# Performance work log

Hardware: AMD Instinct MI355X
Metric: run time of the kernel (lower is better)

## Reference

```python
import jax, jax.numpy as jnp
import numpy as np

BZ, NA, D, R, H, IN, NACT = 64, 64, 128, 3, 4, 96, 20


def setup_inputs() -> dict:
    key = jax.random.key(0)
    ks = jax.random.split(key, 32)

    def lin(k, out_d, in_d):
        return jax.random.normal(k, (out_d, in_d), jnp.float32) / np.sqrt(in_d)

    def linR(k, out_d, in_d):  # stacked per comm round
        return jax.random.normal(k, (R, out_d, in_d), jnp.float32) / np.sqrt(in_d)

    u = jax.random.uniform(ks[0], (R, BZ, NA, NA, 2), jnp.float32, 1e-6, 1.0 - 1e-6)
    gumbel = -jnp.log(-jnp.log(u))  # gumbel(0,1) noise for gumbel-softmax
    return {
        "obs": jax.random.normal(ks[1], (BZ, NA, IN), jnp.float32),
        "hidden": jax.random.normal(ks[2], (BZ, NA, D), jnp.float32),
        "gumbel": gumbel,
        "W_enc": lin(ks[3], D, IN), "b_enc": jnp.zeros((D,), jnp.float32),
        "W_ih": lin(ks[4], 3 * D, D), "W_hh": lin(ks[5], 3 * D, D),
        "b_ih": jnp.zeros((3 * D,), jnp.float32), "b_hh": jnp.zeros((3 * D,), jnp.float32),
        "W_oth": lin(ks[6], D, D), "b_oth": jnp.zeros((D,), jnp.float32),
        "W_m1": lin(ks[7], D, 2 * D), "b_m1": jnp.zeros((D,), jnp.float32),
        "W_m2": lin(ks[8], D, D), "b_m2": jnp.zeros((D,), jnp.float32),
        "W_s1": linR(ks[9], D // 2, 2 * D), "b_s1": jnp.zeros((R, D // 2), jnp.float32),
        "W_s2": linR(ks[10], 2, D // 2), "b_s2": jnp.zeros((R, 2), jnp.float32),
        "Wq": linR(ks[11], D, D), "Wk": linR(ks[12], D, D),
        "Wv": linR(ks[13], D, D), "Wo": linR(ks[14], D, D),
        "W_q1": lin(ks[15], D, 2 * D), "b_q1": jnp.zeros((D,), jnp.float32),
        "W_q2": lin(ks[16], NACT, D), "b_q2": jnp.zeros((NACT,), jnp.float32),
    }


def reference(obs, hidden, gumbel, W_enc, b_enc, W_ih, W_hh, b_ih, b_hh,
              W_oth, b_oth, W_m1, b_m1, W_m2, b_m2, W_s1, b_s1, W_s2, b_s2,
              Wq, Wk, Wv, Wo, W_q1, b_q1, W_q2, b_q2):
    bz, na, _ = obs.shape
    d = W_enc.shape[0]
    # encoder + GRUCell (single step, pytorch gate order r,z,n)
    x = obs @ W_enc.T + b_enc                      # (bz,na,d)
    gx = x @ W_ih.T + b_ih
    gh = hidden @ W_hh.T + b_hh
    xr, xz, xn = jnp.split(gx, 3, -1)
    hr, hz, hn = jnp.split(gh, 3, -1)
    r = jax.nn.sigmoid(xr + hr)
    z = jax.nn.sigmoid(xz + hz)
    nc = jnp.tanh(xn + r * hn)
    h = (1.0 - z) * nc + z * hidden                # (bz,na,d)
    # others encoder on detached hidden
    others = jax.lax.stop_gradient(h) @ W_oth.T + b_oth
    # all-pairs message: [others_j, self_i] -> 2-layer relu MLP
    others_info = jnp.broadcast_to(others[:, None, :, :], (bz, na, na, d))
    self_info = jnp.broadcast_to(h[:, :, None, :], (bz, na, na, d))
    msg_in = jnp.concatenate([others_info, self_info], -1)   # (bz,na,n,2d)
    message = jax.nn.relu(jax.nn.relu(msg_in @ W_m1.T + b_m1) @ W_m2.T + b_m2)
    sched_in = jnp.concatenate([self_info, message], -1)     # (bz,na,n,2d)
    nH, dk = H, d // H
    scale = 1.0 / np.sqrt(dk)
    results = []
    for i in range(R):
        def sched_mlp(xx):
            return jax.nn.relu(xx @ W_s1[i].T + b_s1[i]) @ W_s2[i].T + b_s2[i]
        # directed: symmetrize over the two agent axes of the MLP input
        logits = 0.5 * sched_mlp(sched_in) + 0.5 * sched_mlp(jnp.swapaxes(sched_in, 1, 2))
        y = logits + gumbel[i]
        y_soft = jax.nn.softmax(y, -1)
        y_hard = jax.nn.one_hot(jnp.argmax(y, -1), 2, dtype=y_soft.dtype)
        y_st = y_hard + y_soft - jax.lax.stop_gradient(y_soft)  # straight-through
        adj = y_st[..., 1]                                      # (bz,na,n)
        # multi-head soft attention of agent i over messages j, masked by adj
        q = (h @ Wq[i].T).reshape(bz, na, nH, dk)
        k = (message @ Wk[i].T).reshape(bz, na, na, nH, dk)
        v = (message @ Wv[i].T).reshape(bz, na, na, nH, dk)
        scores = jnp.einsum('bihe,bijhe->bijh', q, k) * scale   # (bz,na,n,H)
        w = jax.nn.softmax(scores, axis=2) * adj[..., None]
        w = w / (jnp.sum(w, axis=2, keepdims=True) + 1e-10)
        att = jnp.einsum('bijh,bijhe->bihe', w, v).reshape(bz, na, d) @ Wo[i].T
        results.append(jax.nn.elu(att))
    aggre = jnp.mean(jnp.stack(results), 0)
    qout = jnp.concatenate([h, aggre], -1)
    qout = jax.nn.relu(qout @ W_q1.T + b_q1) @ W_q2.T + b_q2
    return qout, h
```

## Files before the change

kernel.cpp:

```cpp
#include <hip/hip_runtime.h>
#include <hip/hip_bf16.h>

typedef __hip_bfloat16 bf16;

#define BZc 64
#define NAc 64
#define Dc 128
#define Rc 3
#define Hc 4
#define INc 96
#define NACTc 20

#define WM1_OFF    0
#define WM2_OFF    16384
#define WS1_OFF    32768
#define WM1ST_OFF  57344
#define WS1ST_OFF  73728
#define WENCT_OFF  98304
#define WIHT_OFF   110592
#define WHHT_OFF   159744
#define WOTHT_OFF  208896
#define WQ1T_OFF   225280
#define WQ2T_OFF   258048
#define MH_OFF     260608
#define P_OFF      457216
#define CHUNK_BASE 655360

__global__ void kW(const float* __restrict__ W_m1, const float* __restrict__ W_m2,
                   const float* __restrict__ W_s1, const float* __restrict__ W_enc,
                   const float* __restrict__ W_ih, const float* __restrict__ W_hh,
                   const float* __restrict__ W_oth, const float* __restrict__ W_q1,
                   const float* __restrict__ W_q2, float* __restrict__ ws) {
  int idx = blockIdx.x * blockDim.x + threadIdx.x;
  if (idx < 16384) {
    int dm = idx & 127, c = idx >> 7;
    ws[WM1_OFF + ((c >> 2) * 128 + dm) * 4 + (c & 3)] = W_m1[dm * 256 + c];
  } else if (idx < 32768) {
    int k = idx - 16384;
    int dm = k & 127, c = k >> 7;
    ws[WM2_OFF + ((c >> 2) * 128 + dm) * 4 + (c & 3)] = W_m2[dm * 128 + c];
  } else if (idx < 57344) {
    int k = idx - 32768;
    int r = k >> 13, rem = k & 8191;
    int du = rem & 63, c = rem >> 6;
    ws[WS1_OFF + r * 8192 + ((c >> 2) * 64 + du) * 4 + (c & 3)] =
        W_s1[(r * 64 + du) * 256 + 128 + c];
  } else if (idx < 73728) {
    int k = idx - 57344;
    int dm = k & 127, c = k >> 7;
    ws[WM1ST_OFF + c * 128 + dm] = W_m1[dm * 256 + 128 + c];
  } else if (idx < 98304) {
    int k = idx - 73728;
    int r = k >> 13, rem = k & 8191;
    int du = rem & 63, c = rem >> 6;
    ws[WS1ST_OFF + r * 8192 + c * 64 + du] = W_s1[(r * 64 + du) * 256 + c];
  } else if (idx < 110592) {
    int k = idx - 98304;
    int o = k & 127, c = k >> 7;
    ws[WENCT_OFF + c * 128 + o] = W_enc[o * 96 + c];
  } else if (idx < 159744) {
    int k = idx - 110592;
    int o = k % 384, c = k / 384;
    ws[WIHT_OFF + c * 384 + o] = W_ih[o * 128 + c];
  } else if (idx < 208896) {
    int k = idx - 159744;
    int o = k % 384, c = k / 384;
    ws[WHHT_OFF + c * 384 + o] = W_hh[o * 128 + c];
  } else if (idx < 225280) {
    int k = idx - 208896;
    int o = k & 127, c = k >> 7;
    ws[WOTHT_OFF + c * 128 + o] = W_oth[o * 128 + c];
  } else if (idx < 258048) {
    int k = idx - 225280;
    int o = k & 127, c = k >> 7;
    ws[WQ1T_OFF + c * 128 + o] = W_q1[o * 256 + c];
  } else if (idx < 260608) {
    int k = idx - 258048;
    int o = k % 20, c = k / 20;
    ws[WQ2T_OFF + c * 20 + o] = W_q2[o * 128 + c];
  }
}

__global__ __launch_bounds__(256) void kMP(
    const float* __restrict__ Wq, const float* __restrict__ Wk,
    const float* __restrict__ Wv, const float* __restrict__ Wo,
    float* __restrict__ Mhq, float* __restrict__ Pq) {
  const int bid = blockIdx.x;
  const int which = bid & 1, hh = (bid >> 1) & 3, r = bid >> 3;
  const int t = threadIdx.x;
  __shared__ float A[4096];
  __shared__ float B[4224];
  if (which == 0) {
    for (int k = t; k < 4096; k += 256) {
      int e = k >> 7, c = k & 127;
      A[k] = Wq[(r * 128 + hh * 32 + e) * 128 + c];
      B[k] = Wk[(r * 128 + hh * 32 + e) * 128 + c];
    }
    __syncthreads();
    for (int k = 0; k < 64; ++k) {
      int o = k * 256 + t, c = o >> 7, d = o & 127;
      float a = 0.f;
      #pragma unroll 8
      for (int e = 0; e < 32; ++e) a += A[e * 128 + c] * B[e * 128 + d];
      Mhq[(size_t)(r * 4 + hh) * 16384 + ((c >> 2) * 128 + d) * 4 + (c & 3)] = a;
    }
  } else {
    for (int k = t; k < 4096; k += 256) A[k] = Wv[(r * 128 + hh * 32 + (k >> 7)) * 128 + (k & 127)];
    for (int k = t; k < 4096; k += 256) {
      int dp = k >> 5, e = k & 31;
      B[dp * 33 + e] = Wo[(r * 128 + dp) * 128 + hh * 32 + e];
    }
    __syncthreads();
    for (int k = 0; k < 64; ++k) {
      int o = k * 256 + t, d = o >> 7, dp = o & 127;
      float a = 0.f;
      #pragma unroll 8
      for (int e = 0; e < 32; ++e) a += A[e * 128 + d] * B[dp * 33 + e];
      int kk = hh * 128 + d;
      Pq[(size_t)r * 65536 + ((kk >> 2) * 128 + dp) * 4 + (kk & 3)] = a;
    }
  }
}

__global__ __launch_bounds__(128) void k_enc(
    const float* __restrict__ obs, const float* __restrict__ hidden,
    const float* __restrict__ WencT, const float* __restrict__ b_enc,
    const float* __restrict__ WihT, const float* __restrict__ WhhT,
    const float* __restrict__ b_ih, const float* __restrict__ b_hh,
    const float* __restrict__ WothT, const float* __restrict__ b_oth,
    float* __restrict__ h_f32, float* __restrict__ oth_f32,
    float* __restrict__ out_h, int b0) {
  const int row_l = blockIdx.x, t = threadIdx.x;
  const int row_g = b0 * 64 + row_l;
  __shared__ float obs_s[96], hid_s[128], x_s[128], h_s[128];
  if (t < 96) obs_s[t] = obs[row_g * 96 + t];
  hid_s[t] = hidden[row_g * 128 + t];
  __syncthreads();
  float x = b_enc[t];
  #pragma unroll 8
  for (int c = 0; c < 96; ++c) x += obs_s[c] * WencT[c * 128 + t];
  x_s[t] = x;
  __syncthreads();
  float gxr = b_ih[t], gxz = b_ih[t + 128], gxn = b_ih[t + 256];
  float ghr = b_hh[t], ghz = b_hh[t + 128], ghn = b_hh[t + 256];
  #pragma unroll 4
  for (int c = 0; c < 128; ++c) {
    float xv = x_s[c], hv = hid_s[c];
    const float* wi = WihT + c * 384 + t;
    const float* wh = WhhT + c * 384 + t;
    gxr += xv * wi[0]; gxz += xv * wi[128]; gxn += xv * wi[256];
    ghr += hv * wh[0]; ghz += hv * wh[128]; ghn += hv * wh[256];
  }
  float rg = 1.f / (1.f + expf(-(gxr + ghr)));
  float zg = 1.f / (1.f + expf(-(gxz + ghz)));
  float ng = tanhf(gxn + rg * ghn);
  float hv = (1.f - zg) * ng + zg * hid_s[t];
  h_s[t] = hv;
  h_f32[row_l * 128 + t] = hv;
  out_h[(size_t)row_g * 128 + t] = hv;
  __syncthreads();
  float o = b_oth[t];
  #pragma unroll 4
  for (int c = 0; c < 128; ++c) o += h_s[c] * WothT[c * 128 + t];
  oth_f32[row_l * 128 + t] = o;
}

__global__ __launch_bounds__(320) void k_sp(
    const float* __restrict__ h_f32, const float* __restrict__ Wm1sT,
    const float* __restrict__ b_m1, const float* __restrict__ Ws1sT,
    const float* __restrict__ b_s1,
    float* __restrict__ sp1_g, float* __restrict__ spS_g) {
  const int blk = blockIdx.x, t = threadIdx.x;
  __shared__ float h_s[128];
  if (t < 128) h_s[t] = h_f32[(size_t)blk * 128 + t];
  __syncthreads();
  if (t < 128) {
    float a = b_m1[t];
    #pragma unroll 4
    for (int c = 0; c < 128; ++c) a += h_s[c] * Wm1sT[c * 128 + t];
    sp1_g[(size_t)blk * 128 + t] = a;
  } else {
    const int r = (t - 128) >> 6, du = (t - 128) & 63;
    float a = b_s1[r * 64 + du];
    #pragma unroll 4
    for (int c = 0; c < 128; ++c) a += h_s[c] * Ws1sT[r * 8192 + c * 64 + du];
    spS_g[(size_t)blk * 192 + r * 64 + du] = a;
  }
}

__global__ __launch_bounds__(256) void k_msg(
    const float* __restrict__ oth_f32, const float* __restrict__ sp1_g,
    const float* __restrict__ spS_g, const float* __restrict__ Wm1q,
    const float* __restrict__ Wm2q, const float* __restrict__ b_m2,
    const float* __restrict__ Ws1q, const float* __restrict__ W_s2,
    const float* __restrict__ b_s2,
    bf16* __restrict__ msg_g, float* __restrict__ S_g, int nblk) {
  const int blk = blockIdx.x;
  const int b = blk >> 6;
  const int t = threadIdx.x;
  __shared__ float oth_s[64 * 128];
  __shared__ float tact[64 * 128];
  const int dq = t & 31;
  const int jb = (t >> 5) * 8;
  const int l = t & 63, wv = t >> 6;

  {
    const float* ob = oth_f32 + (size_t)b * 8192;
    for (int k = t; k < 8192; k += 256) oth_s[k] = ob[k];
  }
  const float* spp = sp1_g + (size_t)blk * 128;
  const float sp0 = spp[dq], sp1v = spp[dq + 32], sp2 = spp[dq + 64], sp3 = spp[dq + 96];
  const float* sps = spS_g + (size_t)blk * 192;
  const float spS0 = sps[l], spS1 = sps[64 + l], spS2 = sps[128 + l];
  __syncthreads();
  {
    float a0[8], a1[8], a2[8], a3[8];
    #pragma unroll
    for (int j = 0; j < 8; ++j) { a0[j] = sp0; a1[j] = sp1v; a2[j] = sp2; a3[j] = sp3; }
    const float4* wq = (const float4*)Wm1q;
    for (int c4 = 0; c4 < 32; ++c4) {
      float4 w0 = wq[c4 * 128 + dq];
      float4 w1 = wq[c4 * 128 + dq + 32];
      float4 w2 = wq[c4 * 128 + dq + 64];
      float4 w3 = wq[c4 * 128 + dq + 96];
      #pragma unroll
      for (int j = 0; j < 8; ++j) {
        float4 v = *(const float4*)&oth_s[(jb + j) * 128 + c4 * 4];
        a0[j] += v.x * w0.x; a0[j] += v.y * w0.y; a0[j] += v.z * w0.z; a0[j] += v.w * w0.w;
        a1[j] += v.x * w1.x; a1[j] += v.y * w1.y; a1[j] += v.z * w1.z; a1[j] += v.w * w1.w;
        a2[j] += v.x * w2.x; a2[j] += v.y * w2.y; a2[j] += v.z * w2.z; a2[j] += v.w * w2.w;
        a3[j] += v.x * w3.x; a3[j] += v.y * w3.y; a3[j] += v.z * w3.z; a3[j] += v.w * w3.w;
      }
    }
    #pragma unroll
    for (int j = 0; j < 8; ++j) {
      tact[(jb + j) * 128 + dq]      = fmaxf(a0[j], 0.f);
      tact[(jb + j) * 128 + dq + 32] = fmaxf(a1[j], 0.f);
      tact[(jb + j) * 128 + dq + 64] = fmaxf(a2[j], 0.f);
      tact[(jb + j) * 128 + dq + 96] = fmaxf(a3[j], 0.f);
    }
  }
  __syncthreads();
  {
    float a0[8], a1[8], a2[8], a3[8];
    const float s0 = b_m2[dq], s1 = b_m2[dq + 32], s2 = b_m2[dq + 64], s3 = b_m2[dq + 96];
    #pragma unroll
    for (int j = 0; j < 8; ++j) { a0[j] = s0; a1[j] = s1; a2[j] = s2; a3[j] = s3; }
    const float4* wq = (const float4*)Wm2q;
    for (int c4 = 0; c4 < 32; ++c4) {
      float4 w0 = wq[c4 * 128 + dq];
      float4 w1 = wq[c4 * 128 + dq + 32];
      float4 w2 = wq[c4 * 128 + dq + 64];
      float4 w3 = wq[c4 * 128 + dq + 96];
      #pragma unroll
      for (int j = 0; j < 8; ++j) {
        float4 v = *(const float4*)&tact[(jb + j) * 128 + c4 * 4];
        a0[j] += v.x * w0.x; a0[j] += v.y * w0.y; a0[j] += v.z * w0.z; a0[j] += v.w * w0.w;
        a1[j] += v.x * w1.x; a1[j] += v.y * w1.y; a1[j] += v.z * w1.z; a1[j] += v.w * w1.w;
        a2[j] += v.x * w2.x; a2[j] += v.y * w2.y; a2[j] += v.z * w2.z; a2[j] += v.w * w2.w;
        a3[j] += v.x * w3.x; a3[j] += v.y * w3.y; a3[j] += v.z * w3.z; a3[j] += v.w * w3.w;
      }
    }
    #pragma unroll
    for (int j = 0; j < 8; ++j) {
      float m0 = fmaxf(a0[j], 0.f), m1 = fmaxf(a1[j], 0.f);
      float m2 = fmaxf(a2[j], 0.f), m3 = fmaxf(a3[j], 0.f);
      oth_s[(jb + j) * 128 + dq]      = m0;
      oth_s[(jb + j) * 128 + dq + 32] = m1;
      oth_s[(jb + j) * 128 + dq + 64] = m2;
      oth_s[(jb + j) * 128 + dq + 96] = m3;
      bf16* mg = msg_g + ((size_t)blk * 64 + (jb + j)) * 128 + dq;
      mg[0]  = __float2bfloat16(m0);
      mg[32] = __float2bfloat16(m1);
      mg[64] = __float2bfloat16(m2);
      mg[96] = __float2bfloat16(m3);
    }
  }
  __syncthreads();
  float ua0[16], ua1[16], ua2[16];
  #pragma unroll
  for (int j = 0; j < 16; ++j) { ua0[j] = spS0; ua1[j] = spS1; ua2[j] = spS2; }
  {
    const float4* wq0 = (const float4*)(Ws1q);
    const float4* wq1 = (const float4*)(Ws1q + 8192);
    const float4* wq2 = (const float4*)(Ws1q + 16384);
    for (int c4 = 0; c4 < 32; ++c4) {
      float4 w0 = wq0[c4 * 64 + l];
      float4 w1 = wq1[c4 * 64 + l];
      float4 w2 = wq2[c4 * 64 + l];
      #pragma unroll
      for (int j = 0; j < 16; ++j) {
        float4 v = *(const float4*)&oth_s[(wv * 16 + j) * 128 + c4 * 4];
        ua0[j] += v.x * w0.x + v.y * w0.y + v.z * w0.z + v.w * w0.w;
        ua1[j] += v.x * w1.x + v.y * w1.y + v.z * w1.z + v.w * w1.w;
        ua2[j] += v.x * w2.x + v.y * w2.y + v.z * w2.z + v.w * w2.w;
      }
    }
  }
  {
    const float w2a = W_s2[0 * 64 + l], w2b = W_s2[1 * 64 + l];
    const float bs2a = b_s2[0], bs2b = b_s2[1];
    for (int j = 0; j < 16; ++j) {
      float u = fmaxf(ua0[j], 0.f);
      float v0 = u * w2a, v1 = u * w2b;
      #pragma unroll
      for (int s = 1; s < 64; s <<= 1) {
        v0 += __shfl_xor(v0, s, 64);
        v1 += __shfl_xor(v1, s, 64);
      }
      if (l == 0) {
        float* sp = S_g + (((size_t)0 * nblk + blk) * 64 + (wv * 16 + j)) * 2;
        sp[0] = v0 + bs2a;
        sp[1] = v1 + bs2b;
      }
    }
  }
  {
    const float w2a = W_s2[2 * 64 + l], w2b = W_s2[3 * 64 + l];
    const float bs2a = b_s2[2], bs2b = b_s2[3];
    for (int j = 0; j < 16; ++j) {
      float u = fmaxf(ua1[j], 0.f);
      float v0 = u * w2a, v1 = u * w2b;
      #pragma unroll
      for (int s = 1; s < 64; s <<= 1) {
        v0 += __shfl_xor(v0, s, 64);
        v1 += __shfl_xor(v1, s, 64);
      }
      if (l == 0) {
        float* sp = S_g + (((size_t)1 * nblk + blk) * 64 + (wv * 16 + j)) * 2;
        sp[0] = v0 + bs2a;
        sp[1] = v1 + bs2b;
      }
    }
  }
  {
    const float w2a = W_s2[4 * 64 + l], w2b = W_s2[5 * 64 + l];
    const float bs2a = b_s2[4], bs2b = b_s2[5];
    for (int j = 0; j < 16; ++j) {
      float u = fmaxf(ua2[j], 0.f);
      float v0 = u * w2a, v1 = u * w2b;
      #pragma unroll
      for (int s = 1; s < 64; s <<= 1) {
        v0 += __shfl_xor(v0, s, 64);
        v1 += __shfl_xor(v1, s, 64);
      }
      if (l == 0) {
        float* sp = S_g + (((size_t)2 * nblk + blk) * 64 + (wv * 16 + j)) * 2;
        sp[0] = v0 + bs2a;
        sp[1] = v1 + bs2b;
      }
    }
  }
}

__global__ __launch_bounds__(256) void k_qw(
    const float* __restrict__ h_f32, const float* __restrict__ Mhq,
    float* __restrict__ qW_g, int nblk) {
  const int b = blockIdx.x, r = blockIdx.y, t = threadIdx.x;
  __shared__ float h_s[8192];
  for (int k = t; k < 8192; k += 256) h_s[k] = h_f32[(size_t)b * 8192 + k];
  __syncthreads();
  const int dq = t & 31, ib = (t >> 5) * 8;
  for (int hh = 0; hh < 4; ++hh) {
    float a0[8], a1[8], a2[8], a3[8];
    #pragma unroll
    for (int i = 0; i < 8; ++i) { a0[i] = 0.f; a1[i] = 0.f; a2[i] = 0.f; a3[i] = 0.f; }
    const float4* mq = (const float4*)(Mhq + (size_t)(r * 4 + hh) * 16384);
    for (int c4 = 0; c4 < 32; ++c4) {
      float4 w0 = mq[c4 * 128 + dq];
      float4 w1 = mq[c4 * 128 + dq + 32];
      float4 w2 = mq[c4 * 128 + dq + 64];
      float4 w3 = mq[c4 * 128 + dq + 96];
      #pragma unroll
      for (int i = 0; i < 8; ++i) {
        float4 v = *(const float4*)&h_s[(ib + i) * 128 + c4 * 4];
        a0[i] += v.x * w0.x; a0[i] += v.y * w0.y; a0[i] += v.z * w0.z; a0[i] += v.w * w0.w;
        a1[i] += v.x * w1.x; a1[i] += v.y * w1.y; a1[i] += v.z * w1.z; a1[i] += v.w * w1.w;
        a2[i] += v.x * w2.x; a2[i] += v.y * w2.y; a2[i] += v.z * w2.z; a2[i] += v.w * w2.w;
        a3[i] += v.x * w3.x; a3[i] += v.y * w3.y; a3[i] += v.z * w3.z; a3[i] += v.w * w3.w;
      }
    }
    #pragma unroll
    for (int i = 0; i < 8; ++i) {
      float* qp = qW_g + ((size_t)r * nblk + b * 64 + ib + i) * 512 + hh * 128 + dq;
      qp[0]  = a0[i];
      qp[32] = a1[i];
      qp[64] = a2[i];
      qp[96] = a3[i];
    }
  }
}

__global__ __launch_bounds__(256) void k_attn(
    const bf16* __restrict__ msg_g, const float* __restrict__ S_g,
    const float* __restrict__ gumbel, const float* __restrict__ qW_g,
    float* __restrict__ mw_g, int b0, int nblk) {
  const int blk = blockIdx.x, r = blockIdx.y;
  const int b = blk >> 6, i = blk & 63, t = threadIdx.x;
  __shared__ float msg_s[64][132];
  __shared__ float qW_s[4][132];
  __shared__ float sc_s[320];
  __shared__ float adj_s[64];
  __shared__ float w_s[320];

  {
    const unsigned int* mb = (const unsigned int*)(msg_g + (size_t)blk * 8192);
    for (int k = t; k < 4096; k += 256) {
      unsigned int v = mb[k];
      int j = k >> 6, d2 = (k & 63) * 2;
      msg_s[j][d2]     = __uint_as_float(v << 16);
      msg_s[j][d2 + 1] = __uint_as_float(v & 0xffff0000u);
    }
  }
  for (int o = t; o < 512; o += 256)
    qW_s[o >> 7][o & 127] = qW_g[((size_t)r * nblk + blk) * 512 + o];
  if (t < 64) {
    const int j = t;
    const float* Sij = S_g + (((size_t)r * nblk + blk) * 64 + j) * 2;
    const float* Sji = S_g + (((size_t)r * nblk + b * 64 + j) * 64 + i) * 2;
    const float* g = gumbel + ((((size_t)r * 64 + (b0 + b)) * 64 + i) * 64 + j) * 2;
    float y0 = 0.5f * Sij[0] + 0.5f * Sji[0] + g[0];
    float y1 = 0.5f * Sij[1] + 0.5f * Sji[1] + g[1];
    adj_s[j] = (y1 > y0) ? 1.f : 0.f;
  }
  __syncthreads();
  {
    const int j = t >> 2, hh = t & 3;
    float a = 0.f;
    #pragma unroll
    for (int d4 = 0; d4 < 32; ++d4) {
      float4 mv = *(const float4*)&msg_s[j][d4 * 4];
      float4 qv = *(const float4*)&qW_s[hh][d4 * 4];
      a += mv.x * qv.x + mv.y * qv.y + mv.z * qv.z + mv.w * qv.w;
    }
    sc_s[j * 5 + hh] = a * 0.17677669529663687f;
  }
  __syncthreads();
  {
    const int hh = t >> 6, jj = t & 63;
    float v = sc_s[jj * 5 + hh];
    float mx = v;
    #pragma unroll
    for (int s = 32; s > 0; s >>= 1) mx = fmaxf(mx, __shfl_xor(mx, s, 64));
    float e = expf(v - mx);
    float ad = adj_s[jj];
    float E = e, Em = ad * e;
    #pragma unroll
    for (int s = 32; s > 0; s >>= 1) {
      E += __shfl_xor(E, s, 64);
      Em += __shfl_xor(Em, s, 64);
    }
    w_s[jj * 5 + hh] = ad * e / (Em + 1e-10f * E);
  }
  __syncthreads();
  {
    const int hh0 = t >> 7, d = t & 127;
    float a0 = 0.f, a1 = 0.f;
    for (int j = 0; j < 64; ++j) {
      float m = msg_s[j][d];
      a0 += w_s[j * 5 + hh0] * m;
      a1 += w_s[j * 5 + hh0 + 2] * m;
    }
    float* mp = mw_g + ((size_t)r * nblk + blk) * 512;
    mp[hh0 * 128 + d] = a0;
    mp[(hh0 + 2) * 128 + d] = a1;
  }
}

__global__ __launch_bounds__(256) void k_pv(
    const float* __restrict__ mw_g, const float* __restrict__ Pq,
    float* __restrict__ att_r, int nblk) {
  const int b = blockIdx.x, r = blockIdx.y, t = threadIdx.x;
  const int dq = t & 31, ib = (t >> 5) * 8;
  float a0[8], a1[8], a2[8], a3[8];
  #pragma unroll
  for (int i = 0; i < 8; ++i) { a0[i] = 0.f; a1[i] = 0.f; a2[i] = 0.f; a3[i] = 0.f; }
  const float4* pq = (const float4*)(Pq + (size_t)r * 65536);
  const float* mwb = mw_g + ((size_t)r * nblk + b * 64) * 512;
  for (int c4 = 0; c4 < 128; ++c4) {
    float4 w0 = pq[c4 * 128 + dq];
    float4 w1 = pq[c4 * 128 + dq + 32];
    float4 w2 = pq[c4 * 128 + dq + 64];
    float4 w3 = pq[c4 * 128 + dq + 96];
    #pragma unroll
    for (int i = 0; i < 8; ++i) {
      float4 v = *(const float4*)&mwb[(size_t)(ib + i) * 512 + c4 * 4];
      a0[i] += v.x * w0.x; a0[i] += v.y * w0.y; a0[i] += v.z * w0.z; a0[i] += v.w * w0.w;
      a1[i] += v.x * w1.x; a1[i] += v.y * w1.y; a1[i] += v.z * w1.z; a1[i] += v.w * w1.w;
      a2[i] += v.x * w2.x; a2[i] += v.y * w2.y; a2[i] += v.z * w2.z; a2[i] += v.w * w2.w;
      a3[i] += v.x * w3.x; a3[i] += v.y * w3.y; a3[i] += v.z * w3.z; a3[i] += v.w * w3.w;
    }
  }
  #pragma unroll
  for (int i = 0; i < 8; ++i) {
    float* ap = att_r + ((size_t)r * nblk + b * 64 + ib + i) * 128 + dq;
    ap[0]  = (a0[i] > 0.f) ? a0[i] : expm1f(a0[i]);
    ap[32] = (a1[i] > 0.f) ? a1[i] : expm1f(a1[i]);
    ap[64] = (a2[i] > 0.f) ? a2[i] : expm1f(a2[i]);
    ap[96] = (a3[i] > 0.f) ? a3[i] : expm1f(a3[i]);
  }
}

__global__ __launch_bounds__(128) void k_head(
    const float* __restrict__ h_f32, const float* __restrict__ att_r,
    const float* __restrict__ Wq1T, const float* __restrict__ b_q1,
    const float* __restrict__ Wq2T, const float* __restrict__ b_q2,
    float* __restrict__ out_q, int b0, int nblk) {
  const int blk = blockIdx.x, t = threadIdx.x;
  __shared__ float hi[128], agg[128], u[128];
  hi[t] = h_f32[(size_t)blk * 128 + t];
  agg[t] = (att_r[(size_t)blk * 128 + t] +
            att_r[((size_t)nblk + blk) * 128 + t] +
            att_r[((size_t)2 * nblk + blk) * 128 + t]) * (1.f / 3.f);
  __syncthreads();
  float a = b_q1[t];
  #pragma unroll 4
  for (int c = 0; c < 128; ++c) a += hi[c] * Wq1T[c * 128 + t];
  #pragma unroll 4
  for (int c = 0; c < 128; ++c) a += agg[c] * Wq1T[(128 + c) * 128 + t];
  u[t] = fmaxf(a, 0.f);
  __syncthreads();
  if (t < 20) {
    float a2 = b_q2[t];
    #pragma unroll 4
    for (int c = 0; c < 128; ++c) a2 += u[c] * Wq2T[c * 20 + t];
    out_q[((size_t)b0 * 64 + blk) * 20 + t] = a2;
  }
}

extern "C" void kernel_launch(void* const* d_in, const int* in_sizes, int n_in,
                              void* d_out, int out_size, void* d_ws, size_t ws_size,
                              hipStream_t stream) {
  (void)in_sizes; (void)n_in; (void)out_size;
  const float* obs    = (const float*)d_in[0];
  const float* hidden = (const float*)d_in[1];
  const float* gumb   = (const float*)d_in[2];
  const float* W_enc  = (const float*)d_in[3];
  const float* b_enc  = (const float*)d_in[4];
  const float* W_ih   = (const float*)d_in[5];
  const float* W_hh   = (const float*)d_in[6];
  const float* b_ih   = (const float*)d_in[7];
  const float* b_hh   = (const float*)d_in[8];
  const float* W_oth  = (const float*)d_in[9];
  const float* b_oth  = (const float*)d_in[10];
  const float* W_m1   = (const float*)d_in[11];
  const float* b_m1   = (const float*)d_in[12];
  const float* W_m2   = (const float*)d_in[13];
  const float* b_m2   = (const float*)d_in[14];
  const float* W_s1   = (const float*)d_in[15];
  const float* b_s1   = (const float*)d_in[16];
  const float* W_s2   = (const float*)d_in[17];
  const float* b_s2   = (const float*)d_in[18];
  const float* Wq     = (const float*)d_in[19];
  const float* Wk     = (const float*)d_in[20];
  const float* Wv     = (const float*)d_in[21];
  const float* Wo     = (const float*)d_in[22];
  const float* W_q1   = (const float*)d_in[23];
  const float* b_q1   = (const float*)d_in[24];
  const float* W_q2   = (const float*)d_in[25];
  const float* b_q2   = (const float*)d_in[26];

  float* ws    = (float*)d_ws;
  float* Wm1q  = ws + WM1_OFF;
  float* Wm2q  = ws + WM2_OFF;
  float* Ws1q  = ws + WS1_OFF;
  float* Wm1sT = ws + WM1ST_OFF;
  float* Ws1sT = ws + WS1ST_OFF;
  float* WencT = ws + WENCT_OFF;
  float* WihT  = ws + WIHT_OFF;
  float* WhhT  = ws + WHHT_OFF;
  float* WothT = ws + WOTHT_OFF;
  float* Wq1T  = ws + WQ1T_OFF;
  float* Wq2T  = ws + WQ2T_OFF;
  float* Mhq   = ws + MH_OFF;
  float* Pq    = ws + P_OFF;

  float* out_q = (float*)d_out;
  float* out_h = out_q + BZc * NAc * NACTc;

  int BC = 64;
  while (BC > 1) {
    size_t need = 4ull * CHUNK_BASE + (size_t)BC * 2179072ull;
    if (need <= ws_size) break;
    BC >>= 1;
  }
  const int nblk = BC * 64;
  float* h_f32   = ws + CHUNK_BASE;
  float* oth_f32 = h_f32 + (size_t)BC * 8192;
  float* sp1_g   = oth_f32 + (size_t)BC * 8192;
  float* spS_g   = sp1_g + (size_t)BC * 8192;
  float* S_g     = spS_g + (size_t)BC * 12288;
  float* att_rb  = S_g + (size_t)BC * 24576;
  float* qW_g    = att_rb + (size_t)BC * 24576;
  float* mw_g    = qW_g + (size_t)BC * 98304;
  bf16*  msg_g   = (bf16*)(mw_g + (size_t)BC * 98304);

  kW<<<dim3(1018), dim3(256), 0, stream>>>(W_m1, W_m2, W_s1, W_enc, W_ih, W_hh,
                                           W_oth, W_q1, W_q2, ws);
  kMP<<<dim3(24), dim3(256), 0, stream>>>(Wq, Wk, Wv, Wo, Mhq, Pq);
  for (int b0 = 0; b0 < BZc; b0 += BC) {
    k_enc<<<dim3(nblk), dim3(128), 0, stream>>>(obs, hidden, WencT, b_enc, WihT, WhhT,
                                                b_ih, b_hh, WothT, b_oth,
                                                h_f32, oth_f32, out_h, b0);
    k_sp<<<dim3(nblk), dim3(320), 0, stream>>>(h_f32, Wm1sT, b_m1, Ws1sT, b_s1,
                                               sp1_g, spS_g);
    k_msg<<<dim3(nblk), dim3(256), 0, stream>>>(oth_f32, sp1_g, spS_g, Wm1q,
                                                Wm2q, b_m2, Ws1q,
                                                W_s2, b_s2, msg_g, S_g, nblk);
    k_qw<<<dim3(BC, 3), dim3(256), 0, stream>>>(h_f32, Mhq, qW_g, nblk);
    k_attn<<<dim3(nblk, 3), dim3(256), 0, stream>>>(msg_g, S_g, gumb, qW_g,
                                                    mw_g, b0, nblk);
    k_pv<<<dim3(BC, 3), dim3(256), 0, stream>>>(mw_g, Pq, att_rb, nblk);
    k_head<<<dim3(nblk), dim3(128), 0, stream>>>(h_f32, att_rb, Wq1T, b_q1,
                                                 Wq2T, b_q2, out_q, b0, nblk);
  }
}
```

Measured before the change: 895.7 us.

## Hoist per-batch oth·W_m1 product out of per-agent message kernel

The first message-MLP layer's oth-dependent half, oth·W_m1 over the second half of the input, does not depend on agent i. The code was recomputing it in every (b,i) block. A new per-batch kernel computes this product once and writes it to a buffer. k_msg then only adds the per-agent sp1 term and applies relu, which removes one of its three 64x128x128 matmuls per block. The trade-off is an extra launch and an extra global buffer that every block of a batch reads, plus slightly larger workspace needs.

```diff
diff --git a/kernel.cpp b/kernel.cpp
--- a/kernel.cpp
+++ b/kernel.cpp
@@ -188,9 +188,45 @@
   }
 }
 
+__global__ __launch_bounds__(256) void k_othp(
+    const float* __restrict__ oth_f32, const float* __restrict__ Wm1q,
+    float* __restrict__ othp) {
+  const int b = blockIdx.x, t = threadIdx.x;
+  const int dq = t & 31, jb = (t >> 5) * 8;
+  __shared__ float oth_s[8192];
+  for (int k = t; k < 8192; k += 256) oth_s[k] = oth_f32[(size_t)b * 8192 + k];
+  __syncthreads();
+  float a0[8], a1[8], a2[8], a3[8];
+  #pragma unroll
+  for (int j = 0; j < 8; ++j) { a0[j] = 0.f; a1[j] = 0.f; a2[j] = 0.f; a3[j] = 0.f; }
+  const float4* wq = (const float4*)Wm1q;
+  for (int c4 = 0; c4 < 32; ++c4) {
+    float4 w0 = wq[c4 * 128 + dq];
+    float4 w1 = wq[c4 * 128 + dq + 32];
+    float4 w2 = wq[c4 * 128 + dq + 64];
+    float4 w3 = wq[c4 * 128 + dq + 96];
+    #pragma unroll
+    for (int j = 0; j < 8; ++j) {
+      float4 v = *(const float4*)&oth_s[(jb + j) * 128 + c4 * 4];
+      a0[j] += v.x * w0.x; a0[j] += v.y * w0.y; a0[j] += v.z * w0.z; a0[j] += v.w * w0.w;
+      a1[j] += v.x * w1.x; a1[j] += v.y * w1.y; a1[j] += v.z * w1.z; a1[j] += v.w * w1.w;
+      a2[j] += v.x * w2.x; a2[j] += v.y * w2.y; a2[j] += v.z * w2.z; a2[j] += v.w * w2.w;
+      a3[j] += v.x * w3.x; a3[j] += v.y * w3.y; a3[j] += v.z * w3.z; a3[j] += v.w * w3.w;
+    }
+  }
+  #pragma unroll
+  for (int j = 0; j < 8; ++j) {
+    float* op = othp + (size_t)b * 8192 + (jb + j) * 128 + dq;
+    op[0]  = a0[j];
+    op[32] = a1[j];
+    op[64] = a2[j];
+    op[96] = a3[j];
+  }
+}
+
 __global__ __launch_bounds__(256) void k_msg(
-    const float* __restrict__ oth_f32, const float* __restrict__ sp1_g,
-    const float* __restrict__ spS_g, const float* __restrict__ Wm1q,
+    const float* __restrict__ othp, const float* __restrict__ sp1_g,
+    const float* __restrict__ spS_g,
     const float* __restrict__ Wm2q, const float* __restrict__ b_m2,
     const float* __restrict__ Ws1q, const float* __restrict__ W_s2,
     const float* __restrict__ b_s2,
@@ -198,48 +234,20 @@
   const int blk = blockIdx.x;
   const int b = blk >> 6;
   const int t = threadIdx.x;
-  __shared__ float oth_s[64 * 128];
-  __shared__ float tact[64 * 128];
+  __shared__ float tact_s[64 * 128];
+  __shared__ float msg_s[64 * 128];
   const int dq = t & 31;
   const int jb = (t >> 5) * 8;
   const int l = t & 63, wv = t >> 6;
 
   {
-    const float* ob = oth_f32 + (size_t)b * 8192;
-    for (int k = t; k < 8192; k += 256) oth_s[k] = ob[k];
-  }
-  const float* spp = sp1_g + (size_t)blk * 128;
-  const float sp0 = spp[dq], sp1v = spp[dq + 32], sp2 = spp[dq + 64], sp3 = spp[dq + 96];
+    const float spl = sp1_g[(size_t)blk * 128 + (t & 127)];
+    const float* op = othp + (size_t)b * 8192;
+    for (int k = t; k < 8192; k += 256)
+      tact_s[k] = fmaxf(op[k] + spl, 0.f);
+  }
   const float* sps = spS_g + (size_t)blk * 192;
   const float spS0 = sps[l], spS1 = sps[64 + l], spS2 = sps[128 + l];
-  __syncthreads();
-  {
-    float a0[8], a1[8], a2[8], a3[8];
-    #pragma unroll
-    for (int j = 0; j < 8; ++j) { a0[j] = sp0; a1[j] = sp1v; a2[j] = sp2; a3[j] = sp3; }
-    const float4* wq = (const float4*)Wm1q;
-    for (int c4 = 0; c4 < 32; ++c4) {
-      float4 w0 = wq[c4 * 128 + dq];
-      float4 w1 = wq[c4 * 128 + dq + 32];
-      float4 w2 = wq[c4 * 128 + dq + 64];
-      float4 w3 = wq[c4 * 128 + dq + 96];
-      #pragma unroll
-      for (int j = 0; j < 8; ++j) {
-        float4 v = *(const float4*)&oth_s[(jb + j) * 128 + c4 * 4];
-        a0[j] += v.x * w0.x; a0[j] += v.y * w0.y; a0[j] += v.z * w0.z; a0[j] += v.w * w0.w;
-        a1[j] += v.x * w1.x; a1[j] += v.y * w1.y; a1[j] += v.z * w1.z; a1[j] += v.w * w1.w;
-        a2[j] += v.x * w2.x; a2[j] += v.y * w2.y; a2[j] += v.z * w2.z; a2[j] += v.w * w2.w;
-        a3[j] += v.x * w3.x; a3[j] += v.y * w3.y; a3[j] += v.z * w3.z; a3[j] += v.w * w3.w;
-      }
-    }
-    #pragma unroll
-    for (int j = 0; j < 8; ++j) {
-      tact[(jb + j) * 128 + dq]      = fmaxf(a0[j], 0.f);
-      tact[(jb + j) * 128 + dq + 32] = fmaxf(a1[j], 0.f);
-      tact[(jb + j) * 128 + dq + 64] = fmaxf(a2[j], 0.f);
-      tact[(jb + j) * 128 + dq + 96] = fmaxf(a3[j], 0.f);
-    }
-  }
   __syncthreads();
   {
     float a0[8], a1[8], a2[8], a3[8];
@@ -254,7 +262,7 @@
       float4 w3 = wq[c4 * 128 + dq + 96];
       #pragma unroll
       for (int j = 0; j < 8; ++j) {
-        float4 v = *(const float4*)&tact[(jb + j) * 128 + c4 * 4];
+        float4 v = *(const float4*)&tact_s[(jb + j) * 128 + c4 * 4];
         a0[j] += v.x * w0.x; a0[j] += v.y * w0.y; a0[j] += v.z * w0.z; a0[j] += v.w * w0.w;
         a1[j] += v.x * w1.x; a1[j] += v.y * w1.y; a1[j] += v.z * w1.z; a1[j] += v.w * w1.w;
         a2[j] += v.x * w2.x; a2[j] += v.y * w2.y; a2[j] += v.z * w2.z; a2[j] += v.w * w2.w;
@@ -265,10 +273,10 @@
     for (int j = 0; j < 8; ++j) {
       float m0 = fmaxf(a0[j], 0.f), m1 = fmaxf(a1[j], 0.f);
       float m2 = fmaxf(a2[j], 0.f), m3 = fmaxf(a3[j], 0.f);
-      oth_s[(jb + j) * 128 + dq]      = m0;
-      oth_s[(jb + j) * 128 + dq + 32] = m1;
-      oth_s[(jb + j) * 128 + dq + 64] = m2;
-      oth_s[(jb + j) * 128 + dq + 96] = m3;
+      msg_s[(jb + j) * 128 + dq]      = m0;
+      msg_s[(jb + j) * 128 + dq + 32] = m1;
+      msg_s[(jb + j) * 128 + dq + 64] = m2;
+      msg_s[(jb + j) * 128 + dq + 96] = m3;
       bf16* mg = msg_g + ((size_t)blk * 64 + (jb + j)) * 128 + dq;
       mg[0]  = __float2bfloat16(m0);
       mg[32] = __float2bfloat16(m1);
@@ -290,7 +298,7 @@
       float4 w2 = wq2[c4 * 64 + l];
       #pragma unroll
       for (int j = 0; j < 16; ++j) {
-        float4 v = *(const float4*)&oth_s[(wv * 16 + j) * 128 + c4 * 4];
+        float4 v = *(const float4*)&msg_s[(wv * 16 + j) * 128 + c4 * 4];
         ua0[j] += v.x * w0.x + v.y * w0.y + v.z * w0.z + v.w * w0.w;
         ua1[j] += v.x * w1.x + v.y * w1.y + v.z * w1.z + v.w * w1.w;
         ua2[j] += v.x * w2.x + v.y * w2.y + v.z * w2.z + v.w * w2.w;
@@ -580,14 +588,15 @@
 
   int BC = 64;
   while (BC > 1) {
-    size_t need = 4ull * CHUNK_BASE + (size_t)BC * 2179072ull;
+    size_t need = 4ull * CHUNK_BASE + (size_t)BC * 2211840ull;
     if (need <= ws_size) break;
     BC >>= 1;
   }
   const int nblk = BC * 64;
   float* h_f32   = ws + CHUNK_BASE;
   float* oth_f32 = h_f32 + (size_t)BC * 8192;
-  float* sp1_g   = oth_f32 + (size_t)BC * 8192;
+  float* othp    = oth_f32 + (size_t)BC * 8192;
+  float* sp1_g   = othp + (size_t)BC * 8192;
   float* spS_g   = sp1_g + (size_t)BC * 8192;
   float* S_g     = spS_g + (size_t)BC * 12288;
   float* att_rb  = S_g + (size_t)BC * 24576;
@@ -604,7 +613,8 @@
                                                 h_f32, oth_f32, out_h, b0);
     k_sp<<<dim3(nblk), dim3(320), 0, stream>>>(h_f32, Wm1sT, b_m1, Ws1sT, b_s1,
                                                sp1_g, spS_g);
-    k_msg<<<dim3(nblk), dim3(256), 0, stream>>>(oth_f32, sp1_g, spS_g, Wm1q,
+    k_othp<<<dim3(BC), dim3(256), 0, stream>>>(oth_f32, Wm1q, othp);
+    k_msg<<<dim3(nblk), dim3(256), 0, stream>>>(othp, sp1_g, spS_g,
                                                 Wm2q, b_m2, Ws1q,
                                                 W_s2, b_s2, msg_g, S_g, nblk);
     k_qw<<<dim3(BC, 3), dim3(256), 0, stream>>>(h_f32, Mhq, qW_g, nblk);
```

New measurement: 800.0 us. 1.12x faster.
